# Kernel optimization log

Hardware: AMD Instinct MI355X
Metric: run time of the kernel (lower is better)

Reference implementation:

```python
import jax, jax.numpy as jnp
import numpy as np

EPS = 1e-8
INV_SQRT = 1.0 / np.sqrt(1.0 + EPS)  # 1/sqrt(|k|+eps), |k|=1 for both hyp and sph


def layernorm(x, w, b, eps=1e-5):
    m = jnp.mean(x, axis=-1, keepdims=True)
    v = jnp.mean((x - m) ** 2, axis=-1, keepdims=True)
    return (x - m) * jax.lax.rsqrt(v + eps) * w + b


def setup_inputs() -> dict:
    key = jax.random.key(0)
    B, S, D, H = 4, 1024, 512, 8
    d = D // H
    FF = 2048
    ks = jax.random.split(key, 12)
    s_attn = 1.0 / np.sqrt(d)
    s_d = 1.0 / np.sqrt(D)
    s_ff = 1.0 / np.sqrt(FF)
    return {
        "x": jax.random.normal(ks[0], (B, S, D), jnp.float32),
        "Wq": jax.random.normal(ks[1], (H, d, d), jnp.float32) * s_attn,
        "Wk": jax.random.normal(ks[2], (H, d, d), jnp.float32) * s_attn,
        "Wv": jax.random.normal(ks[3], (H, d, d), jnp.float32) * s_attn,
        "gw": jnp.ones((H, 3), jnp.float32) / 3.0,
        "temp": jnp.ones((H,), jnp.float32),
        "Wo": jax.random.normal(ks[4], (D, D), jnp.float32) * s_d,
        "bo": jnp.zeros((D,), jnp.float32),
        "ln1_w": jnp.ones((D,), jnp.float32),
        "ln1_b": jnp.zeros((D,), jnp.float32),
        "ln2_w": jnp.ones((D,), jnp.float32),
        "ln2_b": jnp.zeros((D,), jnp.float32),
        "W1": jax.random.normal(ks[5], (FF, D), jnp.float32) * s_d,
        "b1": jnp.zeros((FF,), jnp.float32),
        "W2": jax.random.normal(ks[6], (D, FF), jnp.float32) * s_ff,
        "b2": jnp.zeros((D,), jnp.float32),
    }


def reference(x, Wq, Wk, Wv, gw, temp, Wo, bo, ln1_w, ln1_b, ln2_w, ln2_b, W1, b1, W2, b2):
    B, S, D = x.shape
    H = Wq.shape[0]
    d = D // H

    h = layernorm(x, ln1_w, ln1_b)
    xh = h.reshape(B, S, H, d).transpose(0, 2, 1, 3)  # [B,H,S,d]
    # nn.Linear: y = x @ W^T
    q = jnp.einsum("bhsd,hed->bhse", xh, Wq)
    k = jnp.einsum("bhsd,hed->bhse", xh, Wk)
    v = jnp.einsum("bhsd,hed->bhse", xh, Wv)

    qsq = jnp.sum(q * q, axis=-1)  # [B,H,S] == ||q||^2
    ksq = jnp.sum(k * k, axis=-1)
    qk = jnp.einsum("bhsd,bhtd->bhst", q, k)
    # ||q-k||^2 via expansion (same math as sum(diff^2), avoids [B,H,S,S,d])
    dsq = jnp.maximum(qsq[..., :, None] + ksq[..., None, :] - 2.0 * qk, 0.0)
    euc = jnp.sqrt(dsq + EPS)

    denom = (1.0 - qsq)[..., :, None] * (1.0 - ksq)[..., None, :] + EPS
    cosh_arg = jnp.clip(1.0 + 2.0 * dsq / denom, 1.0, 1e6)
    hyp = jnp.arccosh(cosh_arg) * INV_SQRT

    qn = jnp.sqrt(qsq)
    kn = jnp.sqrt(ksq)
    cos_angle = qk / ((qn + EPS)[..., :, None] * (kn + EPS)[..., None, :])
    cos_angle = jnp.clip(cos_angle, -1.0 + EPS, 1.0 - EPS)
    sph = jnp.arccos(cos_angle) * INV_SQRT

    w = jax.nn.softmax(gw, axis=-1)  # [H,3] per-head geometry mixing
    comb = (
        w[:, 0, None, None] * hyp
        + w[:, 1, None, None] * euc
        + w[:, 2, None, None] * sph
    )
    sim = -comb * temp[None, :, None, None]
    attn = jax.nn.softmax(sim, axis=-1)
    out = jnp.einsum("bhst,bhtd->bhsd", attn, v)
    out = out.transpose(0, 2, 1, 3).reshape(B, S, D)
    attn_out = out @ Wo.T + bo

    x = x + attn_out  # dropout=0 (eval)
    h2 = layernorm(x, ln2_w, ln2_b)
    ff = jax.nn.gelu(h2 @ W1.T + b1, approximate=False) @ W2.T + b2
    return x + ff, w
```

## Files before the change

kernel.cpp:

```cpp
#include <hip/hip_runtime.h>
#include <hip/hip_bf16.h>
#include <math.h>

typedef __attribute__((ext_vector_type(4))) float f32x4;
typedef __attribute__((ext_vector_type(8))) short bf16x8;
typedef unsigned short u16;
typedef unsigned int u32;

typedef f32x4  __attribute__((may_alias)) f32x4a;
typedef bf16x8 __attribute__((may_alias)) bf16x8a;
typedef uint2  __attribute__((may_alias)) uint2a;

__device__ __forceinline__ u16 bfbits(float f) {
  union { __hip_bfloat16 h; u16 u; } cv;
  cv.h = __float2bfloat16(f);
  return cv.u;
}
__device__ __forceinline__ float rcp_r(float x)  { return __builtin_amdgcn_rcpf(x); }
__device__ __forceinline__ float sqrt_r(float x) { return __builtin_amdgcn_sqrtf(x); }
__device__ __forceinline__ float log2_r(float x) { return __builtin_amdgcn_logf(x); }
__device__ __forceinline__ float exp2_r(float x) { return __builtin_amdgcn_exp2f(x); }
__device__ __forceinline__ float rsq_r(float x)  { return __builtin_amdgcn_rsqf(x); }
__device__ __forceinline__ u32 cvt_pk_bf16(float lo, float hi) {
  u32 r;
  asm("v_cvt_pk_bf16_f32 %0, %1, %2" : "=v"(r) : "v"(lo), "v"(hi));
  return r;
}
typedef const __attribute__((address_space(1))) unsigned int* gas_t;
typedef __attribute__((address_space(3))) unsigned int* las_t;
__device__ __forceinline__ void gload_lds16(const u16* g, u16* l) {
  __builtin_amdgcn_global_load_lds((gas_t)g, (las_t)l, 16, 0, 0);
}

__global__ __launch_bounds__(256) void convert_weights(
    const float* __restrict__ wq, const float* __restrict__ wk, const float* __restrict__ wv,
    const float* __restrict__ wo, const float* __restrict__ w1, const float* __restrict__ w2,
    u16* __restrict__ owq, u16* __restrict__ owk, u16* __restrict__ owv,
    u16* __restrict__ owo, u16* __restrict__ ow1, u16* __restrict__ ow2) {
  int i = blockIdx.x * 256 + threadIdx.x;
  const float* src; u16* dst; int base;
  if (i < 8192)        { src = wq; dst = owq; base = 0; }
  else if (i < 16384)  { src = wk; dst = owk; base = 8192; }
  else if (i < 24576)  { src = wv; dst = owv; base = 16384; }
  else if (i < 90112)  { src = wo; dst = owo; base = 24576; }
  else if (i < 352256) { src = w1; dst = ow1; base = 90112; }
  else                 { src = w2; dst = ow2; base = 352256; }
  int li = i - base;
  float4 v = reinterpret_cast<const float4*>(src)[li];
  ushort4 o;
  o.x = bfbits(v.x); o.y = bfbits(v.y); o.z = bfbits(v.z); o.w = bfbits(v.w);
  reinterpret_cast<ushort4*>(dst)[li] = o;
}

__global__ __launch_bounds__(128) void ln_kernel(const float* __restrict__ x,
    const float* __restrict__ w, const float* __restrict__ b, u16* __restrict__ out) {
  int row = blockIdx.x, tid = threadIdx.x;
  float4 v = reinterpret_cast<const float4*>(x + row * 512)[tid];
  float s  = v.x + v.y + v.z + v.w;
  float s2 = v.x*v.x + v.y*v.y + v.z*v.z + v.w*v.w;
  #pragma unroll
  for (int o = 32; o > 0; o >>= 1) { s += __shfl_down(s, o); s2 += __shfl_down(s2, o); }
  __shared__ float sm[4];
  if ((tid & 63) == 0) { sm[(tid >> 6)*2] = s; sm[(tid >> 6)*2 + 1] = s2; }
  __syncthreads();
  float ts = sm[0] + sm[2], ts2 = sm[1] + sm[3];
  float mean = ts * (1.f/512.f);
  float var  = ts2 * (1.f/512.f) - mean*mean;
  float rstd = rsq_r(var + 1e-5f);
  float4 wv = reinterpret_cast<const float4*>(w)[tid];
  float4 bv = reinterpret_cast<const float4*>(b)[tid];
  ushort4 o;
  o.x = bfbits((v.x-mean)*rstd*wv.x + bv.x);
  o.y = bfbits((v.y-mean)*rstd*wv.y + bv.y);
  o.z = bfbits((v.z-mean)*rstd*wv.z + bv.z);
  o.w = bfbits((v.w-mean)*rstd*wv.w + bv.w);
  reinterpret_cast<ushort4*>(out + row * 512)[tid] = o;
}

__global__ __launch_bounds__(256) void qkv_kernel(const u16* __restrict__ h1,
    const u16* __restrict__ wqb, const u16* __restrict__ wkb, const u16* __restrict__ wvb,
    u16* __restrict__ q, u16* __restrict__ k, u16* __restrict__ vt,
    float* __restrict__ qsq, float* __restrict__ qrs,
    float* __restrict__ ksq, float* __restrict__ krs) {
  int mt = blockIdx.x, head = blockIdx.y;
  int wave = threadIdx.x >> 6, lane = threadIdx.x & 63;
  int lr = lane & 15, lg = lane >> 4;
  int m0 = mt * 64 + wave * 16;
  const u16* xr = h1 + (m0 + lr) * 512 + head * 64 + lg * 8;
  bf16x8 a0 = *reinterpret_cast<const bf16x8a*>(xr);
  bf16x8 a1 = *reinterpret_cast<const bf16x8a*>(xr + 32);
  int m_base = m0 + 4*lg;
  int bq = m_base >> 10;
  int s_base = m_base & 1023;
  int bh = (bq << 3) + head;
  #pragma unroll 1
  for (int mat = 0; mat < 3; ++mat) {
    const u16* W = (mat == 0 ? wqb : mat == 1 ? wkb : wvb) + head * 4096;
    f32x4 acc[4];
    #pragma unroll
    for (int c = 0; c < 4; c++)
      #pragma unroll
      for (int j = 0; j < 4; j++) acc[c][j] = 0.f;
    #pragma unroll
    for (int c = 0; c < 4; c++) {
      const u16* wr = W + (c*16 + lr) * 64 + lg * 8;
      bf16x8 b0 = *reinterpret_cast<const bf16x8a*>(wr);
      bf16x8 b1 = *reinterpret_cast<const bf16x8a*>(wr + 32);
      acc[c] = __builtin_amdgcn_mfma_f32_16x16x32_bf16(a0, b0, acc[c], 0, 0, 0);
      acc[c] = __builtin_amdgcn_mfma_f32_16x16x32_bf16(a1, b1, acc[c], 0, 0, 0);
    }
    if (mat == 2) {
      #pragma unroll
      for (int c = 0; c < 4; c++)
        #pragma unroll
        for (int j = 0; j < 4; j++)
          vt[(bh*64 + c*16 + lr) * 1024 + s_base + j] = bfbits(acc[c][j]);
    } else {
      u16* dst = (mat == 0 ? q : k);
      float* sq = (mat == 0 ? qsq : ksq);
      float* rs = (mat == 0 ? qrs : krs);
      float ss[4] = {0.f, 0.f, 0.f, 0.f};
      #pragma unroll
      for (int c = 0; c < 4; c++)
        #pragma unroll
        for (int j = 0; j < 4; j++) {
          float vv = acc[c][j];
          dst[(bh*1024 + s_base + j) * 64 + c*16 + lr] = bfbits(vv);
          ss[j] += vv * vv;
        }
      #pragma unroll
      for (int j = 0; j < 4; j++) {
        #pragma unroll
        for (int o = 1; o < 16; o <<= 1) ss[j] += __shfl_xor(ss[j], o);
      }
      if (lr == 0) {
        #pragma unroll
        for (int j = 0; j < 4; j++) {
          float v = ss[j];
          int idx = bh*1024 + s_base + j;
          sq[idx] = v;
          rs[idx] = rsq_r(v);
        }
      }
    }
  }
}

__global__ __launch_bounds__(512, 6) void attn_kernel(
    const u16* __restrict__ q, const u16* __restrict__ k, const u16* __restrict__ vt,
    const float* __restrict__ qsqA, const float* __restrict__ qrsA,
    const float* __restrict__ ksqA, const float* __restrict__ krsA,
    const float* __restrict__ gw, const float* __restrict__ temp,
    u16* __restrict__ attnb) {
  int bh = blockIdx.y;
  int b = bh >> 3, head = bh & 7;
  int tid = threadIdx.x;
  int wave = tid >> 6;
  int wq = wave & 1;
  int split = wave >> 1;
  int lane = tid & 63;
  int lr = lane & 15, lg = lane >> 4;
  int q0 = blockIdx.x * 32 + wq * 16;

  const u16* qp = q  + bh * 65536;
  const u16* kp = k  + bh * 65536;
  const u16* vp = vt + bh * 65536;

  __shared__ float ks_s[1024], rkn_s[1024];
  __shared__ __align__(16) u16 umem[5120];
  u16* pw = umem + wave * 640;

  for (int i = tid; i < 1024; i += 512) {
    ks_s[i]  = ksqA[(bh << 10) + i];
    rkn_s[i] = krsA[(bh << 10) + i];
  }
  __syncthreads();

  float g0 = gw[head*3], g1 = gw[head*3+1], g2 = gw[head*3+2];
  float gm = fmaxf(g0, fmaxf(g1, g2));
  float e0 = __expf(g0-gm), e1 = __expf(g1-gm), e2 = __expf(g2-gm);
  float gi = rcp_r(e0 + e1 + e2);
  float tp = temp[head];
  const float LOG2E = 1.4426950408889634f;
  float chn = -e0*gi*tp;
  float cen = -e1*gi*tp*LOG2E;
  float csn = -e2*gi*tp*LOG2E;

  const u16* qr = qp + (q0 + lr) * 64 + lg * 8;
  bf16x8 aq0 = *reinterpret_cast<const bf16x8a*>(qr);
  bf16x8 aq1 = *reinterpret_cast<const bf16x8a*>(qr + 32);
  float qs  = qsqA[(bh << 10) + q0 + lr];
  float omq = 1.f - qs;
  float rqn = qrsA[(bh << 10) + q0 + lr];

  f32x4 acc[4];
  #pragma unroll
  for (int c = 0; c < 4; c++)
    #pragma unroll
    for (int j = 0; j < 4; j++) acc[c][j] = 0.f;
  float psum0 = 0.f, psum1 = 0.f;

  for (int it = 0; it < 8; ++it) {
    int t0 = split * 256 + it * 32;
    const u16* kr = kp + (t0 + lr) * 64 + lg * 8;
    bf16x8 k00 = *reinterpret_cast<const bf16x8a*>(kr);
    bf16x8 k01 = *reinterpret_cast<const bf16x8a*>(kr + 32);
    bf16x8 k10 = *reinterpret_cast<const bf16x8a*>(kr + 1024);
    bf16x8 k11 = *reinterpret_cast<const bf16x8a*>(kr + 1024 + 32);
    f32x4 s0, s1;
    #pragma unroll
    for (int j = 0; j < 4; j++) { s0[j] = 0.f; s1[j] = 0.f; }
    s0 = __builtin_amdgcn_mfma_f32_16x16x32_bf16(k00, aq0, s0, 0, 0, 0);
    s0 = __builtin_amdgcn_mfma_f32_16x16x32_bf16(k01, aq1, s0, 0, 0, 0);
    s1 = __builtin_amdgcn_mfma_f32_16x16x32_bf16(k10, aq0, s1, 0, 0, 0);
    s1 = __builtin_amdgcn_mfma_f32_16x16x32_bf16(k11, aq1, s1, 0, 0, 0);

    f32x4 kq0 = *reinterpret_cast<const f32x4a*>(&ks_s[t0 + 4*lg]);
    f32x4 kq1 = *reinterpret_cast<const f32x4a*>(&ks_s[t0 + 16 + 4*lg]);
    f32x4 rk0 = *reinterpret_cast<const f32x4a*>(&rkn_s[t0 + 4*lg]);
    f32x4 rk1 = *reinterpret_cast<const f32x4a*>(&rkn_s[t0 + 16 + 4*lg]);

    float pv0[4], pv1[4];
    #pragma unroll
    for (int tc = 0; tc < 2; tc++) {
      f32x4 sv = tc ? s1 : s0;
      f32x4 kq = tc ? kq1 : kq0;
      f32x4 rk = tc ? rk1 : rk0;
      float* pv = tc ? pv1 : pv0;
      #pragma unroll
      for (int j = 0; j < 4; j++) {
        float qk  = sv[j];
        float ksj = kq[j];
        float dsq = fmaxf(fmaf(qk, -2.f, qs + ksj), 0.f);
        float euc = sqrt_r(dsq + 1e-8f);
        float den = fmaf(omq, 1.f - ksj, 1e-8f);
        float u   = (dsq + dsq) * rcp_r(den);
        u = fminf(fmaxf(u, 0.f), 999999.f);
        float hyp2 = log2_r((u + 1.f) + sqrt_r(u * (u + 2.f)));
        float ca = qk * rqn * rk[j];
        ca = fminf(fmaxf(ca, -1.f), 1.f);
        float aa = fabsf(ca);
        float pp = fmaf(aa, -0.0187293f, 0.0742610f);
        pp = fmaf(aa, pp, -0.2121144f);
        pp = fmaf(aa, pp, 1.5707288f);
        float rr = sqrt_r(1.f - aa) * pp;
        float sph = ca < 0.f ? 3.14159265358979f - rr : rr;
        float sim2 = fmaf(chn, hyp2, fmaf(cen, euc, csn * sph));
        float p = exp2_r(sim2);
        if (tc) psum1 += p; else psum0 += p;
        pv[j] = p;
      }
    }
    u32 w0 = cvt_pk_bf16(pv0[0], pv0[1]);
    u32 w1 = cvt_pk_bf16(pv0[2], pv0[3]);
    u32 w2 = cvt_pk_bf16(pv1[0], pv1[1]);
    u32 w3 = cvt_pk_bf16(pv1[2], pv1[3]);
    *reinterpret_cast<uint2a*>(pw + lr*40 + 4*lg)      = make_uint2(w0, w1);
    *reinterpret_cast<uint2a*>(pw + lr*40 + 16 + 4*lg) = make_uint2(w2, w3);
    bf16x8 pa = *reinterpret_cast<const bf16x8a*>(pw + lr*40 + lg*8);
    #pragma unroll
    for (int c = 0; c < 4; c++) {
      bf16x8 av = *reinterpret_cast<const bf16x8a*>(vp + (c*16 + lr)*1024 + t0 + lg*8);
      acc[c] = __builtin_amdgcn_mfma_f32_16x16x32_bf16(av, pa, acc[c], 0, 0, 0);
    }
  }

  float lt = psum0 + psum1;
  lt += __shfl_xor(lt, 16);
  lt += __shfl_xor(lt, 32);

  float* fa = (float*)umem;
  __syncthreads();
  #pragma unroll 1
  for (int s = 1; s <= 3; ++s) {
    int base = (wq*64 + lane)*20;
    if (split == s) {
      #pragma unroll
      for (int c = 0; c < 4; c++)
        *reinterpret_cast<f32x4a*>(fa + base + c*4) = acc[c];
      fa[base + 16] = lt;
    }
    __syncthreads();
    if (split == 0) {
      #pragma unroll
      for (int c = 0; c < 4; c++)
        acc[c] += *reinterpret_cast<const f32x4a*>(fa + base + c*4);
      lt += fa[base + 16];
    }
    __syncthreads();
  }
  if (split == 0) {
    float rl = rcp_r(lt);
    #pragma unroll
    for (int c = 0; c < 4; c++) {
      ushort4 st;
      st.x = bfbits(acc[c][0]*rl); st.y = bfbits(acc[c][1]*rl);
      st.z = bfbits(acc[c][2]*rl); st.w = bfbits(acc[c][3]*rl);
      *reinterpret_cast<ushort4*>(
          &attnb[(size_t)((b << 10) + q0 + lr) * 512 + head*64 + c*16 + 4*lg]) = st;
    }
  }
}

template<int K, int KS, int BN, int MODE>
__global__ __launch_bounds__(256, 4) void gemm_kernel(
    const u16* __restrict__ X, const u16* __restrict__ W,
    const float* __restrict__ bias, const float* __restrict__ res,
    float* __restrict__ outf, float* __restrict__ outf2, u16* __restrict__ outb,
    const float* __restrict__ gw, float* __restrict__ wout) {
  constexpr int NS = (MODE == 1) ? 2048 : 512;
  constexpr int WN = BN / 2;
  constexpr int NFC = WN / 16;
  __shared__ u16 As[64 * 32];
  __shared__ u16 Bs[BN * 32];
  int tid = threadIdx.x;
  int wave = tid >> 6, lane = tid & 63;
  int lr = lane & 15, lg = lane >> 4;
  int wr = wave >> 1, wc = wave & 1;
  int m0 = blockIdx.x * 64, n0 = blockIdx.y * BN;
  const u16* Xp = X;
  const u16* Wp = W;
  if constexpr (MODE == 3) { Xp += blockIdx.z * (KS/2); Wp += blockIdx.z * (KS/2); }
  f32x4 acc[2][NFC];
  #pragma unroll
  for (int fr = 0; fr < 2; fr++)
    #pragma unroll
    for (int fc = 0; fc < NFC; fc++)
      #pragma unroll
      for (int j = 0; j < 4; j++) acc[fr][fc][j] = 0.f;
  int arow = tid >> 2;
  int acol = ((tid & 3) ^ (arow & 3)) << 3;
  const u16* Ag = Xp + (size_t)(m0 + arow) * KS + acol;
  u16* Al = As + wave * 512;
  const u16* Bg0 = Wp + (size_t)(n0 + arow) * KS + acol;
  u16* Bl0 = Bs + wave * 512;
  const u16* Bg1 = nullptr; u16* Bl1 = nullptr;
  if constexpr (BN == 128) {
    int c1 = 256 + tid, r1 = c1 >> 2;
    int s1 = ((c1 & 3) ^ (r1 & 3)) << 3;
    Bg1 = Wp + (size_t)(n0 + r1) * KS + s1;
    Bl1 = Bs + 2048 + wave * 512;
  }
  int rdcol = ((lg ^ (lr & 3)) << 3);
  for (int k0 = 0; k0 < K; k0 += 32) {
    __syncthreads();
    gload_lds16(Ag + k0, Al);
    if (BN != 32 || tid < 128) gload_lds16(Bg0 + k0, Bl0);
    if constexpr (BN == 128) gload_lds16(Bg1 + k0, Bl1);
    __syncthreads();
    bf16x8 af[2], bfr[NFC];
    #pragma unroll
    for (int fr = 0; fr < 2; fr++)
      af[fr] = *reinterpret_cast<const bf16x8a*>(As + (wr*32 + fr*16 + lr)*32 + rdcol);
    #pragma unroll
    for (int fc = 0; fc < NFC; fc++)
      bfr[fc] = *reinterpret_cast<const bf16x8a*>(Bs + (wc*WN + fc*16 + lr)*32 + rdcol);
    #pragma unroll
    for (int fr = 0; fr < 2; fr++)
      #pragma unroll
      for (int fc = 0; fc < NFC; fc++)
        acc[fr][fc] = __builtin_amdgcn_mfma_f32_16x16x32_bf16(af[fr], bfr[fc], acc[fr][fc], 0, 0, 0);
  }
  float* po = nullptr;
  if constexpr (MODE == 3) po = blockIdx.z ? outf2 : outf;
  #pragma unroll
  for (int fr = 0; fr < 2; fr++)
    #pragma unroll
    for (int fc = 0; fc < NFC; fc++) {
      int col = n0 + wc*WN + fc*16 + lr;
      float bb = (MODE == 3) ? 0.f : bias[col];
      #pragma unroll
      for (int j = 0; j < 4; j++) {
        int row = m0 + wr*32 + fr*16 + 4*lg + j;
        float v = acc[fr][fc][j] + bb;
        if constexpr (MODE == 0) {
          outf[(size_t)row*NS + col] = v + res[(size_t)row*NS + col];
        } else if constexpr (MODE == 1) {
          float t = v * fmaf(v*v, 0.035677408137f, 0.7978845608f);
          float g = v * rcp_r(1.f + exp2_r(-2.8853900817779268f * t));
          outb[(size_t)row*NS + col] = bfbits(g);
        } else {
          po[(size_t)row*512 + col] = v;
        }
      }
    }
  (void)gw; (void)wout;
}

__global__ __launch_bounds__(256) void ff2_combine(
    const float* __restrict__ p0, const float* __restrict__ p1,
    const float* __restrict__ bias, const float* __restrict__ res,
    float* __restrict__ out, const float* __restrict__ gw, float* __restrict__ wout) {
  int i = blockIdx.x * 256 + threadIdx.x;
  float4 a = reinterpret_cast<const float4*>(p0)[i];
  float4 b = reinterpret_cast<const float4*>(p1)[i];
  float4 r = reinterpret_cast<const float4*>(res)[i];
  int col4 = (i & 127) << 2;
  float4 bb = *reinterpret_cast<const float4*>(bias + col4);
  float4 o;
  o.x = a.x + b.x + r.x + bb.x;
  o.y = a.y + b.y + r.y + bb.y;
  o.z = a.z + b.z + r.z + bb.z;
  o.w = a.w + b.w + r.w + bb.w;
  reinterpret_cast<float4*>(out)[i] = o;
  if (blockIdx.x == 0 && threadIdx.x < 8) {
    int h = threadIdx.x;
    float a0 = gw[h*3], a1 = gw[h*3+1], a2 = gw[h*3+2];
    float m = fmaxf(a0, fmaxf(a1, a2));
    float x0 = __expf(a0-m), x1 = __expf(a1-m), x2 = __expf(a2-m);
    float inv = rcp_r(x0 + x1 + x2);
    wout[h*3+0] = x0*inv; wout[h*3+1] = x1*inv; wout[h*3+2] = x2*inv;
  }
}

extern "C" void kernel_launch(void* const* d_in, const int* in_sizes, int n_in,
                              void* d_out, int out_size, void* d_ws, size_t ws_size,
                              hipStream_t stream) {
  const float* x    = (const float*)d_in[0];
  const float* Wq   = (const float*)d_in[1];
  const float* Wk   = (const float*)d_in[2];
  const float* Wv   = (const float*)d_in[3];
  const float* gw   = (const float*)d_in[4];
  const float* temp = (const float*)d_in[5];
  const float* Wo   = (const float*)d_in[6];
  const float* bo   = (const float*)d_in[7];
  const float* ln1w = (const float*)d_in[8];
  const float* ln1b = (const float*)d_in[9];
  const float* ln2w = (const float*)d_in[10];
  const float* ln2b = (const float*)d_in[11];
  const float* W1   = (const float*)d_in[12];
  const float* b1   = (const float*)d_in[13];
  const float* W2   = (const float*)d_in[14];
  const float* b2   = (const float*)d_in[15];

  char* ws = (char*)d_ws;
  u16*  wqb  = (u16*)(ws + 0);
  u16*  wkb  = (u16*)(ws + 65536);
  u16*  wvb  = (u16*)(ws + 131072);
  u16*  wob  = (u16*)(ws + 196608);
  u16*  w1b  = (u16*)(ws + 720896);
  u16*  w2b  = (u16*)(ws + 2818048);
  u16*  h1b  = (u16*)(ws + 4915200);
  u16*  qb   = (u16*)(ws + 9109504);
  u16*  kb   = (u16*)(ws + 13303808);
  u16*  vtb  = (u16*)(ws + 17498112);
  float* qsq = (float*)(ws + 21692416);
  float* ksq = (float*)(ws + 21823488);
  float* qrs = (float*)(ws + 21954560);
  float* krs = (float*)(ws + 22085632);
  u16*  attnb= (u16*)(ws + 22478848);
  float* x1  = (float*)(ws + 26673152);
  u16*  h2b  = (u16*)(ws + 35061760);
  float* p1f = (float*)(ws + 35061760);
  u16*  gb   = (u16*)(ws + 4915200);

  float* outf = (float*)d_out;
  float* wout = outf + 4096*512;

  convert_weights<<<2400, 256, 0, stream>>>(Wq, Wk, Wv, Wo, W1, W2,
                                            wqb, wkb, wvb, wob, w1b, w2b);
  ln_kernel<<<4096, 128, 0, stream>>>(x, ln1w, ln1b, h1b);
  qkv_kernel<<<dim3(64, 8), 256, 0, stream>>>(h1b, wqb, wkb, wvb, qb, kb, vtb,
                                              qsq, qrs, ksq, krs);
  attn_kernel<<<dim3(32, 32), 512, 0, stream>>>(qb, kb, vtb, qsq, qrs,
                                                ksq, krs, gw, temp, attnb);
  gemm_kernel<512, 512, 64, 0><<<dim3(64, 8), 256, 0, stream>>>(
      attnb, wob, bo, x, x1, nullptr, nullptr, nullptr, nullptr);
  ln_kernel<<<4096, 128, 0, stream>>>(x1, ln2w, ln2b, h2b);
  gemm_kernel<512, 512, 128, 1><<<dim3(64, 16), 256, 0, stream>>>(
      h2b, w1b, b1, nullptr, nullptr, nullptr, gb, nullptr, nullptr);
  gemm_kernel<1024, 2048, 64, 3><<<dim3(64, 8, 2), 256, 0, stream>>>(
      gb, w2b, nullptr, nullptr, outf, p1f, nullptr, nullptr, nullptr);
  ff2_combine<<<2048, 256, 0, stream>>>(outf, p1f, b2, x1, outf, gw, wout);
}
```

Before: 222.9 us.

## Precompute hyperbolic reciprocals per row and enlarge GEMM tiles for FFN

The QKV kernel now also writes 1/(1-||q||^2) and 1/(1-||k||^2), so the attention inner loop replaces a per-pair reciprocal with two multiplies. It also drops the eps terms inside sqrt and the denominator, and the attention launch bound changes from 6 to 4. The GEMM template gains a BM parameter and generalised loaders, so the FF1 and FF2 GEMMs use 128-row tiles with more MFMA work per wave. That means fewer blocks and more registers per thread. Dropping eps slightly changes numerics near the ball boundary.

```diff
diff --git a/kernel.cpp b/kernel.cpp
--- a/kernel.cpp
+++ b/kernel.cpp
@@ -80,8 +80,8 @@
 __global__ __launch_bounds__(256) void qkv_kernel(const u16* __restrict__ h1,
     const u16* __restrict__ wqb, const u16* __restrict__ wkb, const u16* __restrict__ wvb,
     u16* __restrict__ q, u16* __restrict__ k, u16* __restrict__ vt,
-    float* __restrict__ qsq, float* __restrict__ qrs,
-    float* __restrict__ ksq, float* __restrict__ krs) {
+    float* __restrict__ qsq, float* __restrict__ qom, float* __restrict__ qrs,
+    float* __restrict__ ksq, float* __restrict__ kom, float* __restrict__ krs) {
   int mt = blockIdx.x, head = blockIdx.y;
   int wave = threadIdx.x >> 6, lane = threadIdx.x & 63;
   int lr = lane & 15, lg = lane >> 4;
@@ -118,6 +118,7 @@
     } else {
       u16* dst = (mat == 0 ? q : k);
       float* sq = (mat == 0 ? qsq : ksq);
+      float* om = (mat == 0 ? qom : kom);
       float* rs = (mat == 0 ? qrs : krs);
       float ss[4] = {0.f, 0.f, 0.f, 0.f};
       #pragma unroll
@@ -139,6 +140,7 @@
           float v = ss[j];
           int idx = bh*1024 + s_base + j;
           sq[idx] = v;
+          om[idx] = rcp_r(1.f - v);
           rs[idx] = rsq_r(v);
         }
       }
@@ -146,10 +148,10 @@
   }
 }
 
-__global__ __launch_bounds__(512, 6) void attn_kernel(
+__global__ __launch_bounds__(512, 4) void attn_kernel(
     const u16* __restrict__ q, const u16* __restrict__ k, const u16* __restrict__ vt,
-    const float* __restrict__ qsqA, const float* __restrict__ qrsA,
-    const float* __restrict__ ksqA, const float* __restrict__ krsA,
+    const float* __restrict__ qsqA, const float* __restrict__ qomA, const float* __restrict__ qrsA,
+    const float* __restrict__ ksqA, const float* __restrict__ komA, const float* __restrict__ krsA,
     const float* __restrict__ gw, const float* __restrict__ temp,
     u16* __restrict__ attnb) {
   int bh = blockIdx.y;
@@ -166,12 +168,13 @@
   const u16* kp = k  + bh * 65536;
   const u16* vp = vt + bh * 65536;
 
-  __shared__ float ks_s[1024], rkn_s[1024];
+  __shared__ float ks_s[1024], kom_s[1024], rkn_s[1024];
   __shared__ __align__(16) u16 umem[5120];
   u16* pw = umem + wave * 640;
 
   for (int i = tid; i < 1024; i += 512) {
     ks_s[i]  = ksqA[(bh << 10) + i];
+    kom_s[i] = komA[(bh << 10) + i];
     rkn_s[i] = krsA[(bh << 10) + i];
   }
   __syncthreads();
@@ -189,9 +192,9 @@
   const u16* qr = qp + (q0 + lr) * 64 + lg * 8;
   bf16x8 aq0 = *reinterpret_cast<const bf16x8a*>(qr);
   bf16x8 aq1 = *reinterpret_cast<const bf16x8a*>(qr + 32);
-  float qs  = qsqA[(bh << 10) + q0 + lr];
-  float omq = 1.f - qs;
-  float rqn = qrsA[(bh << 10) + q0 + lr];
+  float qs   = qsqA[(bh << 10) + q0 + lr];
+  float qom2 = 2.f * qomA[(bh << 10) + q0 + lr];
+  float rqn  = qrsA[(bh << 10) + q0 + lr];
 
   f32x4 acc[4];
   #pragma unroll
@@ -217,6 +220,8 @@
 
     f32x4 kq0 = *reinterpret_cast<const f32x4a*>(&ks_s[t0 + 4*lg]);
     f32x4 kq1 = *reinterpret_cast<const f32x4a*>(&ks_s[t0 + 16 + 4*lg]);
+    f32x4 ko0 = *reinterpret_cast<const f32x4a*>(&kom_s[t0 + 4*lg]);
+    f32x4 ko1 = *reinterpret_cast<const f32x4a*>(&kom_s[t0 + 16 + 4*lg]);
     f32x4 rk0 = *reinterpret_cast<const f32x4a*>(&rkn_s[t0 + 4*lg]);
     f32x4 rk1 = *reinterpret_cast<const f32x4a*>(&rkn_s[t0 + 16 + 4*lg]);
 
@@ -225,18 +230,19 @@
     for (int tc = 0; tc < 2; tc++) {
       f32x4 sv = tc ? s1 : s0;
       f32x4 kq = tc ? kq1 : kq0;
+      f32x4 ko = tc ? ko1 : ko0;
       f32x4 rk = tc ? rk1 : rk0;
       float* pv = tc ? pv1 : pv0;
       #pragma unroll
       for (int j = 0; j < 4; j++) {
         float qk  = sv[j];
-        float ksj = kq[j];
-        float dsq = fmaxf(fmaf(qk, -2.f, qs + ksj), 0.f);
-        float euc = sqrt_r(dsq + 1e-8f);
-        float den = fmaf(omq, 1.f - ksj, 1e-8f);
-        float u   = (dsq + dsq) * rcp_r(den);
+        float dsq = fmaxf(fmaf(qk, -2.f, qs + kq[j]), 0.f);
+        float euc = sqrt_r(dsq);
+        float u   = dsq * qom2 * ko[j];
         u = fminf(fmaxf(u, 0.f), 999999.f);
-        float hyp2 = log2_r((u + 1.f) + sqrt_r(u * (u + 2.f)));
+        float u2 = u + u;
+        float sr = sqrt_r(fmaf(u, u, u2));
+        float hyp2 = log2_r((u + 1.f) + sr);
         float ca = qk * rqn * rk[j];
         ca = fminf(fmaxf(ca, -1.f), 1.f);
         float aa = fabsf(ca);
@@ -302,76 +308,89 @@
   }
 }
 
-template<int K, int KS, int BN, int MODE>
-__global__ __launch_bounds__(256, 4) void gemm_kernel(
+template<int K, int KS, int BM, int BN, int MODE>
+__global__ __launch_bounds__(256, 2) void gemm_kernel(
     const u16* __restrict__ X, const u16* __restrict__ W,
     const float* __restrict__ bias, const float* __restrict__ res,
-    float* __restrict__ outf, float* __restrict__ outf2, u16* __restrict__ outb,
-    const float* __restrict__ gw, float* __restrict__ wout) {
-  constexpr int NS = (MODE == 1) ? 2048 : 512;
-  constexpr int WN = BN / 2;
+    float* __restrict__ outf, float* __restrict__ outf2, u16* __restrict__ outb) {
+  constexpr int NS  = (MODE == 1) ? 2048 : 512;
+  constexpr int WM  = (BM == 128 && BN == 128) ? 64 : 32;
+  constexpr int WN  = (BN == 128 || BM == 128) ? 64 : 32;
+  constexpr int NFR = WM / 16;
   constexpr int NFC = WN / 16;
-  __shared__ u16 As[64 * 32];
+  constexpr int NWC = BN / WN;
+  constexpr int ACH = (BM * 4) / 256;
+  constexpr int BCH = (BN * 4) / 256;
+  __shared__ u16 As[BM * 32];
   __shared__ u16 Bs[BN * 32];
   int tid = threadIdx.x;
   int wave = tid >> 6, lane = tid & 63;
   int lr = lane & 15, lg = lane >> 4;
-  int wr = wave >> 1, wc = wave & 1;
-  int m0 = blockIdx.x * 64, n0 = blockIdx.y * BN;
+  int wr = (NWC == 2) ? (wave >> 1) : wave;
+  int wc = (NWC == 2) ? (wave & 1) : 0;
+  int m0 = blockIdx.x * BM, n0 = blockIdx.y * BN;
   const u16* Xp = X;
   const u16* Wp = W;
-  if constexpr (MODE == 3) { Xp += blockIdx.z * (KS/2); Wp += blockIdx.z * (KS/2); }
-  f32x4 acc[2][NFC];
-  #pragma unroll
-  for (int fr = 0; fr < 2; fr++)
+  if constexpr (MODE == 3) { Xp += blockIdx.z * K; Wp += blockIdx.z * K; }
+  f32x4 acc[NFR][NFC];
+  #pragma unroll
+  for (int fr = 0; fr < NFR; fr++)
     #pragma unroll
     for (int fc = 0; fc < NFC; fc++)
       #pragma unroll
       for (int j = 0; j < 4; j++) acc[fr][fc][j] = 0.f;
-  int arow = tid >> 2;
-  int acol = ((tid & 3) ^ (arow & 3)) << 3;
-  const u16* Ag = Xp + (size_t)(m0 + arow) * KS + acol;
-  u16* Al = As + wave * 512;
-  const u16* Bg0 = Wp + (size_t)(n0 + arow) * KS + acol;
-  u16* Bl0 = Bs + wave * 512;
-  const u16* Bg1 = nullptr; u16* Bl1 = nullptr;
-  if constexpr (BN == 128) {
-    int c1 = 256 + tid, r1 = c1 >> 2;
-    int s1 = ((c1 & 3) ^ (r1 & 3)) << 3;
-    Bg1 = Wp + (size_t)(n0 + r1) * KS + s1;
-    Bl1 = Bs + 2048 + wave * 512;
+  const u16* Ag[ACH]; u16* Al[ACH];
+  const u16* Bg[BCH]; u16* Bl[BCH];
+  #pragma unroll
+  for (int i = 0; i < ACH; i++) {
+    int cb = i * 256 + wave * 64;
+    int c  = cb + lane;
+    int row = c >> 2;
+    int col = ((c & 3) ^ (row & 3)) << 3;
+    Ag[i] = Xp + (size_t)(m0 + row) * KS + col;
+    Al[i] = As + cb * 8;
+  }
+  #pragma unroll
+  for (int i = 0; i < BCH; i++) {
+    int cb = i * 256 + wave * 64;
+    int c  = cb + lane;
+    int row = c >> 2;
+    int col = ((c & 3) ^ (row & 3)) << 3;
+    Bg[i] = Wp + (size_t)(n0 + row) * KS + col;
+    Bl[i] = Bs + cb * 8;
   }
   int rdcol = ((lg ^ (lr & 3)) << 3);
   for (int k0 = 0; k0 < K; k0 += 32) {
     __syncthreads();
-    gload_lds16(Ag + k0, Al);
-    if (BN != 32 || tid < 128) gload_lds16(Bg0 + k0, Bl0);
-    if constexpr (BN == 128) gload_lds16(Bg1 + k0, Bl1);
+    #pragma unroll
+    for (int i = 0; i < ACH; i++) gload_lds16(Ag[i] + k0, Al[i]);
+    #pragma unroll
+    for (int i = 0; i < BCH; i++) gload_lds16(Bg[i] + k0, Bl[i]);
     __syncthreads();
-    bf16x8 af[2], bfr[NFC];
-    #pragma unroll
-    for (int fr = 0; fr < 2; fr++)
-      af[fr] = *reinterpret_cast<const bf16x8a*>(As + (wr*32 + fr*16 + lr)*32 + rdcol);
+    bf16x8 af[NFR], bf_[NFC];
+    #pragma unroll
+    for (int fr = 0; fr < NFR; fr++)
+      af[fr] = *reinterpret_cast<const bf16x8a*>(As + (wr*WM + fr*16 + lr)*32 + rdcol);
     #pragma unroll
     for (int fc = 0; fc < NFC; fc++)
-      bfr[fc] = *reinterpret_cast<const bf16x8a*>(Bs + (wc*WN + fc*16 + lr)*32 + rdcol);
-    #pragma unroll
-    for (int fr = 0; fr < 2; fr++)
+      bf_[fc] = *reinterpret_cast<const bf16x8a*>(Bs + (wc*WN + fc*16 + lr)*32 + rdcol);
+    #pragma unroll
+    for (int fr = 0; fr < NFR; fr++)
       #pragma unroll
       for (int fc = 0; fc < NFC; fc++)
-        acc[fr][fc] = __builtin_amdgcn_mfma_f32_16x16x32_bf16(af[fr], bfr[fc], acc[fr][fc], 0, 0, 0);
+        acc[fr][fc] = __builtin_amdgcn_mfma_f32_16x16x32_bf16(af[fr], bf_[fc], acc[fr][fc], 0, 0, 0);
   }
   float* po = nullptr;
   if constexpr (MODE == 3) po = blockIdx.z ? outf2 : outf;
   #pragma unroll
-  for (int fr = 0; fr < 2; fr++)
+  for (int fr = 0; fr < NFR; fr++)
     #pragma unroll
     for (int fc = 0; fc < NFC; fc++) {
       int col = n0 + wc*WN + fc*16 + lr;
       float bb = (MODE == 3) ? 0.f : bias[col];
       #pragma unroll
       for (int j = 0; j < 4; j++) {
-        int row = m0 + wr*32 + fr*16 + 4*lg + j;
+        int row = m0 + wr*WM + fr*16 + 4*lg + j;
         float v = acc[fr][fc][j] + bb;
         if constexpr (MODE == 0) {
           outf[(size_t)row*NS + col] = v + res[(size_t)row*NS + col];
@@ -384,7 +403,6 @@
         }
       }
     }
-  (void)gw; (void)wout;
 }
 
 __global__ __launch_bounds__(256) void ff2_combine(
@@ -446,8 +464,10 @@
   u16*  vtb  = (u16*)(ws + 17498112);
   float* qsq = (float*)(ws + 21692416);
   float* ksq = (float*)(ws + 21823488);
-  float* qrs = (float*)(ws + 21954560);
-  float* krs = (float*)(ws + 22085632);
+  float* qom = (float*)(ws + 21954560);
+  float* qrs = (float*)(ws + 22085632);
+  float* kom = (float*)(ws + 22216704);
+  float* krs = (float*)(ws + 22347776);
   u16*  attnb= (u16*)(ws + 22478848);
   float* x1  = (float*)(ws + 26673152);
   u16*  h2b  = (u16*)(ws + 35061760);
@@ -461,15 +481,15 @@
                                             wqb, wkb, wvb, wob, w1b, w2b);
   ln_kernel<<<4096, 128, 0, stream>>>(x, ln1w, ln1b, h1b);
   qkv_kernel<<<dim3(64, 8), 256, 0, stream>>>(h1b, wqb, wkb, wvb, qb, kb, vtb,
-                                              qsq, qrs, ksq, krs);
-  attn_kernel<<<dim3(32, 32), 512, 0, stream>>>(qb, kb, vtb, qsq, qrs,
-                                                ksq, krs, gw, temp, attnb);
-  gemm_kernel<512, 512, 64, 0><<<dim3(64, 8), 256, 0, stream>>>(
-      attnb, wob, bo, x, x1, nullptr, nullptr, nullptr, nullptr);
+                                              qsq, qom, qrs, ksq, kom, krs);
+  attn_kernel<<<dim3(32, 32), 512, 0, stream>>>(qb, kb, vtb, qsq, qom, qrs,
+                                                ksq, kom, krs, gw, temp, attnb);
+  gemm_kernel<512, 512, 64, 64, 0><<<dim3(64, 8), 256, 0, stream>>>(
+      attnb, wob, bo, x, x1, nullptr, nullptr);
   ln_kernel<<<4096, 128, 0, stream>>>(x1, ln2w, ln2b, h2b);
-  gemm_kernel<512, 512, 128, 1><<<dim3(64, 16), 256, 0, stream>>>(
-      h2b, w1b, b1, nullptr, nullptr, nullptr, gb, nullptr, nullptr);
-  gemm_kernel<1024, 2048, 64, 3><<<dim3(64, 8, 2), 256, 0, stream>>>(
-      gb, w2b, nullptr, nullptr, outf, p1f, nullptr, nullptr, nullptr);
+  gemm_kernel<512, 512, 128, 128, 1><<<dim3(32, 16), 256, 0, stream>>>(
+      h2b, w1b, b1, nullptr, nullptr, nullptr, gb);
+  gemm_kernel<1024, 2048, 128, 64, 3><<<dim3(32, 8, 2), 256, 0, stream>>>(
+      gb, w2b, nullptr, nullptr, outf, p1f, nullptr);
   ff2_combine<<<2048, 256, 0, stream>>>(outf, p1f, b2, x1, outf, gw, wout);
 }
```

New measurement: 224.5 us. About the same (+0.7%).
